# Kernel optimization log

Measured on AMD Instinct MI355X. Metric: run time of the kernel, lower is better.

Reference implementation:

```python
import jax, jax.numpy as jnp
import numpy as np

B, C, I = 4096, 256, 16          # nodes, channels (num_features), per-channel irrep dim (lmax=3)
K3, K2, K1 = 23, 4, 1            # num symmetric-contraction paths per correlation order


def setup_inputs() -> dict:
    key = jax.random.key(0)
    ks = jax.random.split(key, 8)
    return {
        "node_feats": jax.random.normal(ks[0], (B, C, I), jnp.float32),
        "U3": jax.random.normal(ks[1], (I, I, I, K3), jnp.float32),  # fixed CG basis, corr=3
        "U2": jax.random.normal(ks[2], (I, I, K2), jnp.float32),     # fixed CG basis, corr=2
        "U1": jax.random.normal(ks[3], (I, K1), jnp.float32),        # fixed CG basis, corr=1
        "w3": jax.random.normal(ks[4], (C, K3), jnp.float32),        # per-channel weights, corr=3
        "w2": jax.random.normal(ks[5], (C, K2), jnp.float32),
        "w1": jax.random.normal(ks[6], (C, K1), jnp.float32),
        "W_lin": jax.random.normal(ks[7], (C, C), jnp.float32),      # o3.Linear (scalars) weight
    }


def reference(node_feats, U3, U2, U1, w3, w2, w1, W_lin):
    """MACE symmetric contraction (ProductBasisBlock), vectorized over channels.

    Per-channel math (correlation = 3):
      out = einsum('pqik,k,bi->bpq', U3, w3[c], x[:,c])          # main
      c2  = einsum('pqk,k->pq', U2, w2[c]); out = einsum('bpi,bi->bp', c2+out, x[:,c])
      c1  = einsum('pk,k->p',  U1, w1[c]); out = einsum('bi,bi->b',  c1+out, x[:,c])
    The Python-level per-channel loop is replaced by a channel axis c in the einsums.
    """
    x = node_feats                                            # (B, C, I)
    # --- main contraction at correlation order 3 ---
    U3w = jnp.einsum('pqik,ck->cpqi', U3, w3)                 # (C, I, I, I)
    out = jnp.einsum('cpqi,bci->bcpq', U3w, x)                # (B, C, I, I)
    # --- corr = 2 ---
    c2 = jnp.einsum('pik,ck->cpi', U2, w2)                    # (C, I, I)
    out = jnp.einsum('bcpi,bci->bcp', c2[None] + out, x)      # (B, C, I)
    # --- corr = 1 ---
    c1 = jnp.einsum('ik,ck->ci', U1, w1)                      # (C, I)
    out = jnp.einsum('bci,bci->bc', c1[None] + out, x)        # (B, C)
    # --- o3.Linear on the scalar (0e) outputs: x @ W with 1/sqrt(fan_in) path norm ---
    inv_sqrt_fan_in = 1.0 / np.sqrt(C).astype(np.float32)
    return jnp.einsum('bc,cd->bd', out, W_lin) * inv_sqrt_fan_in
```

## Files before the change

kernel.cpp:

```cpp
#include <hip/hip_runtime.h>


#define B_NODES 4096
#define C_CH    256
#define K3      23
#define K2      4

#define KSTEPS   7
#define KB_ELEMS (KSTEPS * 64 * 8)
#define KB_U32   (KB_ELEMS / 2)

#define TILES_PER_WAVE 8

typedef short    short8 __attribute__((ext_vector_type(8)));
typedef float    f32x4  __attribute__((ext_vector_type(4)));
typedef unsigned u32x4  __attribute__((ext_vector_type(4)));

static constexpr size_t OFF_BF_BYTES = 0;
static constexpr size_t OFF_ST_BYTES = (size_t)C_CH * KB_ELEMS * 2;

__device__ inline unsigned short f2bf_rne(float f) {
  unsigned u = __builtin_bit_cast(unsigned, f);
  unsigned r = u + 0x7FFFu + ((u >> 16) & 1u);
  return (unsigned short)(r >> 16);
}

#define F2U(f) __builtin_bit_cast(unsigned, (f))
#define PK2(YH, YL) __builtin_amdgcn_perm(F2U(YH), F2U(YL), 0x07060302u)

__global__ __launch_bounds__(256) void precompute_bfrag(
    const float* __restrict__ U3, const float* __restrict__ U2,
    const float* __restrict__ U1, const float* __restrict__ w3,
    const float* __restrict__ w2, const float* __restrict__ w1,
    unsigned int* __restrict__ bfrag_u32) {
  const int c = blockIdx.x;
  const int t = threadIdx.x;

  __shared__ float su3w[4096];
  for (int l = t; l < 4096; l += 256) {
    float a = 0.f;
#pragma unroll
    for (int k3 = 0; k3 < K3; ++k3)
      a += U3[(size_t)l * K3 + k3] * w3[c * K3 + k3];
    su3w[l] = a;
  }
  __syncthreads();

  const int lane = t >> 2;
  const int jj   = (t & 3) * 2;
  const int p = lane & 15, g = lane >> 4;

#pragma unroll
  for (int s = 0; s < 4; ++s) {
    const int q = 2 * s + (g >> 1);
    float v0 = 0.f, v1 = 0.f;
#pragma unroll
    for (int e = 0; e < 2; ++e) {
      const int i = (g & 1) * 8 + jj + e;
      float a = 0.f;
      if (q < i)
        a = su3w[(p * 16 + q) * 16 + i] + su3w[(p * 16 + i) * 16 + q];
      else if (q == i)
        a = su3w[(p * 16 + q) * 16 + q];
      if (e == 0) v0 = a; else v1 = a;
    }
    bfrag_u32[(size_t)c * KB_U32 + s * 256 + t] =
        (unsigned)f2bf_rne(v0) | ((unsigned)f2bf_rne(v1) << 16);
  }

#pragma unroll
  for (int s = 4; s < 6; ++s) {
    const int q = 8 + (s - 4) * 4 + g;
    float v0 = 0.f, v1 = 0.f;
#pragma unroll
    for (int e = 0; e < 2; ++e) {
      const int i = 8 + jj + e;
      float a = 0.f;
      if (q < i)
        a = su3w[(p * 16 + q) * 16 + i] + su3w[(p * 16 + i) * 16 + q];
      else if (q == i)
        a = su3w[(p * 16 + q) * 16 + q];
      if (e == 0) v0 = a; else v1 = a;
    }
    bfrag_u32[(size_t)c * KB_U32 + s * 256 + t] =
        (unsigned)f2bf_rne(v0) | ((unsigned)f2bf_rne(v1) << 16);
  }

  {
    float v0 = 0.f, v1 = 0.f;
#pragma unroll
    for (int e = 0; e < 2; ++e) {
      const int k = 256 + g * 8 + jj + e;
      float a = 0.f;
      if (k < 272) {
        const int q = k - 256;
#pragma unroll
        for (int k2 = 0; k2 < K2; ++k2)
          a += U2[(size_t)(p * 16 + q) * K2 + k2] * w2[c * K2 + k2];
      } else if (k == 272) {
        a = U1[p] * w1[c];
      }
      if (e == 0) v0 = a; else v1 = a;
    }
    bfrag_u32[(size_t)c * KB_U32 + 6 * 256 + t] =
        (unsigned)f2bf_rne(v0) | ((unsigned)f2bf_rne(v1) << 16);
  }
}


#define QSTEP8(BF, XQ, H0, H1, H2, H3, H4, H5, H6, H7, ACC)                    \
  __builtin_amdgcn_mfma_f32_16x16x32_bf16((BF),                                \
      __builtin_bit_cast(short8, (u32x4){                                      \
          PK2((XQ) * (H1), (XQ) * (H0)), PK2((XQ) * (H3), (XQ) * (H2)),        \
          PK2((XQ) * (H5), (XQ) * (H4)), PK2((XQ) * (H7), (XQ) * (H6))}),      \
      (ACC), 0, 0, 0)

#define TILE_BODY(X0, X1, X2, X3, Tc)                                          \
  do {                                                                         \
    const float xh0 = ghi ? (X2).x : (X0).x;                                   \
    const float xh1 = ghi ? (X2).y : (X0).y;                                   \
    const float xh2 = ghi ? (X2).z : (X0).z;                                   \
    const float xh3 = ghi ? (X2).w : (X0).w;                                   \
    const float xh4 = ghi ? (X3).x : (X1).x;                                   \
    const float xh5 = ghi ? (X3).y : (X1).y;                                   \
    const float xh6 = ghi ? (X3).z : (X1).z;                                   \
    const float xh7 = ghi ? (X3).w : (X1).w;                                   \
    const float xq0 = gq ? (X0).y : (X0).x;                                    \
    const float xq1 = gq ? (X0).w : (X0).z;                                    \
    const float xq2 = gq ? (X1).y : (X1).x;                                    \
    const float xq3 = gq ? (X1).w : (X1).z;                                    \
    const float xq4 = (g == 0) ? (X2).x                                        \
                   : (g == 1) ? (X2).y                                         \
                   : (g == 2) ? (X2).z : (X2).w;                  \
    const float xq5 = (g == 0) ? (X3).x                                        \
                   : (g == 1) ? (X3).y                                         \
                   : (g == 2) ? (X3).z : (X3).w;                  \
    f32x4 acc  = (f32x4){0.f, 0.f, 0.f, 0.f};                                  \
    f32x4 acc2 = (f32x4){0.f, 0.f, 0.f, 0.f};                                  \
    acc  = QSTEP8(bf0, xq0, xh0, xh1, xh2, xh3, xh4, xh5, xh6, xh7, acc);      \
    acc2 = QSTEP8(bf1, xq1, xh0, xh1, xh2, xh3, xh4, xh5, xh6, xh7, acc2);     \
    acc  = QSTEP8(bf2, xq2, xh0, xh1, xh2, xh3, xh4, xh5, xh6, xh7, acc);      \
    acc2 = QSTEP8(bf3, xq3, xh0, xh1, xh2, xh3, xh4, xh5, xh6, xh7, acc2);     \
    acc  = QSTEP8(bf4, xq4, (X2).x, (X2).y, (X2).z, (X2).w,                    \
                  (X3).x, (X3).y, (X3).z, (X3).w, acc);                        \
    acc2 = QSTEP8(bf5, xq5, (X2).x, (X2).y, (X2).z, (X2).w,                    \
                  (X3).x, (X3).y, (X3).z, (X3).w, acc2);                       \
    {                                                                          \
      const float y0 = glin ? xh0 : cst;                                       \
      const float y1 = glin ? xh1 : 0.f;                                       \
      const float y2 = glin ? xh2 : 0.f;                                       \
      const float y3 = glin ? xh3 : 0.f;                                       \
      const float y4 = glin ? xh4 : 0.f;                                       \
      const float y5 = glin ? xh5 : 0.f;                                       \
      const float y6 = glin ? xh6 : 0.f;                                       \
      const float y7 = glin ? xh7 : 0.f;                                       \
      acc = __builtin_amdgcn_mfma_f32_16x16x32_bf16(bf6,                       \
          __builtin_bit_cast(short8, (u32x4){PK2(y1, y0), PK2(y3, y2),         \
                                             PK2(y5, y4), PK2(y7, y6)}),       \
          acc, 0, 0, 0);                                                       \
    }                                                                          \
    acc = acc + acc2;                                                          \
    const float4 xs = (g & 2) ? ((g & 1) ? (X3) : (X2))                        \
                              : ((g & 1) ? (X1) : (X0));                       \
    float v = acc[0] * xs.x + acc[1] * xs.y + acc[2] * xs.z + acc[3] * xs.w;   \
    v += __shfl_xor(v, 16);                                                    \
    v += __shfl_xor(v, 32);                                                    \
    if (g == 0) sTrow[(Tc) * 16 + n] = v;                                      \
  } while (0)

__global__ __launch_bounds__(256)
__attribute__((amdgpu_waves_per_eu(2, 4)))
void contract_mfma(
    const float* __restrict__ x, const short8* __restrict__ bfragv,
    float* __restrict__ sT) {
  const int c0  = blockIdx.x * 4;
  const int nb0 = blockIdx.y * (TILES_PER_WAVE * 16);
  const int t   = threadIdx.x;
  const int w = t >> 6, lane = t & 63, n = lane & 15, g = lane >> 4;
  const int ch = c0 + w;

  const short8* bp = bfragv + (size_t)ch * (KSTEPS * 64);
  const short8 bf0 = bp[0 * 64 + lane];
  const short8 bf1 = bp[1 * 64 + lane];
  const short8 bf2 = bp[2 * 64 + lane];
  const short8 bf3 = bp[3 * 64 + lane];
  const short8 bf4 = bp[4 * 64 + lane];
  const short8 bf5 = bp[5 * 64 + lane];
  const short8 bf6 = bp[6 * 64 + lane];

  const bool  ghi  = (g & 1) != 0;
  const bool  gq   = ((g >> 1) & 1) != 0;
  const bool  glin = (g < 2);
  const float cst  = (g == 2) ? 1.0f : 0.0f;
  float* sTrow = sT + (size_t)ch * B_NODES + nb0;

  const float* xb = x + (size_t)(nb0 + n) * (C_CH * 16) + (size_t)ch * 16;
  const size_t tstride = (size_t)16 * C_CH * 16;

  float4 a0, a1, a2, a3, b0, b1, b2, b3;
  {
    const float4* p = (const float4*)xb;
    a0 = p[0]; a1 = p[1]; a2 = p[2]; a3 = p[3];
  }

#pragma unroll
  for (int TT = 0; TT < TILES_PER_WAVE / 2; ++TT) {
    {
      const float4* p = (const float4*)(xb + (size_t)(2 * TT + 1) * tstride);
      b0 = p[0]; b1 = p[1]; b2 = p[2]; b3 = p[3];
    }
    TILE_BODY(a0, a1, a2, a3, 2 * TT);
    if (TT + 1 < TILES_PER_WAVE / 2) {
      const float4* p = (const float4*)(xb + (size_t)(2 * TT + 2) * tstride);
      a0 = p[0]; a1 = p[1]; a2 = p[2]; a3 = p[3];
    }
    TILE_BODY(b0, b1, b2, b3, 2 * TT + 1);
  }
}

__global__ __launch_bounds__(256) void linear_kernel(
    const float* __restrict__ sT, const float* __restrict__ W,
    float* __restrict__ out) {
  const int b0 = blockIdx.x * 64;
  const int d0 = blockIdx.y * 64;
  const int t  = threadIdx.x;
  const int tx = t & 15;
  const int ty = t >> 4;

  __shared__ float As[16][64];
  __shared__ float Bs[16][64];
  float acc[4][4] = {};

  for (int k0 = 0; k0 < C_CH; k0 += 16) {
    const int kk  = t >> 6;
    const int col = t & 63;
#pragma unroll
    for (int r = 0; r < 4; ++r) {
      As[kk + r * 4][col] = sT[(size_t)(k0 + kk + r * 4) * B_NODES + b0 + col];
      Bs[kk + r * 4][col] = W[(size_t)(k0 + kk + r * 4) * C_CH + d0 + col];
    }
    __syncthreads();
#pragma unroll
    for (int k = 0; k < 16; ++k) {
      float a[4], bv[4];
#pragma unroll
      for (int i = 0; i < 4; ++i) a[i] = As[k][ty * 4 + i];
#pragma unroll
      for (int j = 0; j < 4; ++j) bv[j] = Bs[k][tx * 4 + j];
#pragma unroll
      for (int i = 0; i < 4; ++i)
#pragma unroll
        for (int j = 0; j < 4; ++j) acc[i][j] += a[i] * bv[j];
    }
    __syncthreads();
  }

#pragma unroll
  for (int i = 0; i < 4; ++i) {
    float4 v = make_float4(acc[i][0] * 0.0625f, acc[i][1] * 0.0625f,
                           acc[i][2] * 0.0625f, acc[i][3] * 0.0625f);
    *(float4*)(out + (size_t)(b0 + ty * 4 + i) * C_CH + d0 + tx * 4) = v;
  }
}

extern "C" void kernel_launch(void* const* d_in, const int* in_sizes, int n_in,
                              void* d_out, int out_size, void* d_ws, size_t ws_size,
                              hipStream_t stream) {
  const float* x  = (const float*)d_in[0];
  const float* U3 = (const float*)d_in[1];
  const float* U2 = (const float*)d_in[2];
  const float* U1 = (const float*)d_in[3];
  const float* w3 = (const float*)d_in[4];
  const float* w2 = (const float*)d_in[5];
  const float* w1 = (const float*)d_in[6];
  const float* Wl = (const float*)d_in[7];

  unsigned int* bfrag = (unsigned int*)((char*)d_ws + OFF_BF_BYTES);
  float*        sT    = (float*)((char*)d_ws + OFF_ST_BYTES);
  float*        out   = (float*)d_out;

  precompute_bfrag<<<dim3(C_CH), dim3(256), 0, stream>>>(
      U3, U2, U1, w3, w2, w1, bfrag);
  contract_mfma<<<dim3(C_CH / 4, B_NODES / (TILES_PER_WAVE * 16)), dim3(256), 0, stream>>>(
      x, (const short8*)bfrag, sT);
  linear_kernel<<<dim3(B_NODES / 64, C_CH / 64), dim3(256), 0, stream>>>(sT, Wl, out);
}
```

Baseline: 151.3 us.

## Stage node-feature tiles into LDS via async global_load_lds with swizzle

The contraction kernel now issues all eight per-wave tile loads up front as direct global-to-LDS 16-byte transfers, using an XOR-swizzled layout. Each tile is processed after a staged s_waitcnt vmcnt that counts down the outstanding loads. Per-tile results are held in registers and written once at the end. The aim is deeper memory-level parallelism and coalesced loads, in place of the per-lane strided float4 register double-buffer, at the cost of extra LDS usage and LDS read traffic.

```diff
diff --git a/kernel.cpp b/kernel.cpp
--- a/kernel.cpp
+++ b/kernel.cpp
@@ -27,6 +27,12 @@
 
 #define F2U(f) __builtin_bit_cast(unsigned, (f))
 #define PK2(YH, YL) __builtin_amdgcn_perm(F2U(YH), F2U(YL), 0x07060302u)
+
+__device__ __forceinline__ void stage16(const float* g, float* l) {
+  __builtin_amdgcn_global_load_lds(
+      (const __attribute__((address_space(1))) unsigned int*)g,
+      (__attribute__((address_space(3))) unsigned int*)l, 16, 0, 0);
+}
 
 __global__ __launch_bounds__(256) void precompute_bfrag(
     const float* __restrict__ U3, const float* __restrict__ U2,
@@ -115,7 +121,7 @@
           PK2((XQ) * (H5), (XQ) * (H4)), PK2((XQ) * (H7), (XQ) * (H6))}),      \
       (ACC), 0, 0, 0)
 
-#define TILE_BODY(X0, X1, X2, X3, Tc)                                          \
+#define TILE_BODY(X0, X1, X2, X3, VOUT)                                        \
   do {                                                                         \
     const float xh0 = ghi ? (X2).x : (X0).x;                                   \
     const float xh1 = ghi ? (X2).y : (X0).y;                                   \
@@ -160,12 +166,24 @@
           acc, 0, 0, 0);                                                       \
     }                                                                          \
     acc = acc + acc2;                                                          \
-    const float4 xs = (g & 2) ? ((g & 1) ? (X3) : (X2))                        \
-                              : ((g & 1) ? (X1) : (X0));                       \
-    float v = acc[0] * xs.x + acc[1] * xs.y + acc[2] * xs.z + acc[3] * xs.w;   \
+    const float4 xs4 = (g & 2) ? ((g & 1) ? (X3) : (X2))                       \
+                               : ((g & 1) ? (X1) : (X0));                      \
+    float v = acc[0] * xs4.x + acc[1] * xs4.y + acc[2] * xs4.z + acc[3] * xs4.w;\
     v += __shfl_xor(v, 16);                                                    \
     v += __shfl_xor(v, 32);                                                    \
-    if (g == 0) sTrow[(Tc) * 16 + n] = v;                                      \
+    (VOUT) = v;                                                                \
+  } while (0)
+
+#define TILE_AT(T, NREM, VOUT)                                                 \
+  do {                                                                         \
+    asm volatile("s_waitcnt vmcnt(" #NREM ")" ::: "memory");                   \
+    __builtin_amdgcn_sched_barrier(0);                                         \
+    const float* lw = lbase + (T) * 256;                                       \
+    const float4 X0 = *(const float4*)(lw + n16 + sw0);                        \
+    const float4 X1 = *(const float4*)(lw + n16 + sw1);                        \
+    const float4 X2 = *(const float4*)(lw + n16 + sw2);                        \
+    const float4 X3 = *(const float4*)(lw + n16 + sw3);                        \
+    TILE_BODY(X0, X1, X2, X3, VOUT);                                           \
   } while (0)
 
 __global__ __launch_bounds__(256)
@@ -179,6 +197,8 @@
   const int w = t >> 6, lane = t & 63, n = lane & 15, g = lane >> 4;
   const int ch = c0 + w;
 
+  __shared__ float xstage[4][TILES_PER_WAVE][256];
+
   const short8* bp = bfragv + (size_t)ch * (KSTEPS * 64);
   const short8 bf0 = bp[0 * 64 + lane];
   const short8 bf1 = bp[1 * 64 + lane];
@@ -194,27 +214,44 @@
   const float cst  = (g == 2) ? 1.0f : 0.0f;
   float* sTrow = sT + (size_t)ch * B_NODES + nb0;
 
-  const float* xb = x + (size_t)(nb0 + n) * (C_CH * 16) + (size_t)ch * 16;
+  const int nl = lane >> 2;
+  const int sl = lane & 3;
+  const int cg = sl ^ ((nl >> 1) & 3);
   const size_t tstride = (size_t)16 * C_CH * 16;
-
-  float4 a0, a1, a2, a3, b0, b1, b2, b3;
-  {
-    const float4* p = (const float4*)xb;
-    a0 = p[0]; a1 = p[1]; a2 = p[2]; a3 = p[3];
-  }
-
-#pragma unroll
-  for (int TT = 0; TT < TILES_PER_WAVE / 2; ++TT) {
-    {
-      const float4* p = (const float4*)(xb + (size_t)(2 * TT + 1) * tstride);
-      b0 = p[0]; b1 = p[1]; b2 = p[2]; b3 = p[3];
-    }
-    TILE_BODY(a0, a1, a2, a3, 2 * TT);
-    if (TT + 1 < TILES_PER_WAVE / 2) {
-      const float4* p = (const float4*)(xb + (size_t)(2 * TT + 2) * tstride);
-      a0 = p[0]; a1 = p[1]; a2 = p[2]; a3 = p[3];
-    }
-    TILE_BODY(b0, b1, b2, b3, 2 * TT + 1);
+  const float* gs = x + (size_t)(nb0 + nl) * (C_CH * 16) + (size_t)ch * 16
+                      + (size_t)cg * 4;
+  float* lbase = &xstage[w][0][0];
+#pragma unroll
+  for (int T = 0; T < TILES_PER_WAVE; ++T)
+    stage16(gs + (size_t)T * tstride, lbase + T * 256);
+  __builtin_amdgcn_sched_barrier(0);
+
+  const int n16 = n * 16;
+  const int swz = (n >> 1) & 3;
+  const int sw0 = (0 ^ swz) << 2;
+  const int sw1 = (1 ^ swz) << 2;
+  const int sw2 = (2 ^ swz) << 2;
+  const int sw3 = (3 ^ swz) << 2;
+
+  float v0, v1, v2, v3, v4, v5, v6, v7;
+  TILE_AT(0, 7, v0);
+  TILE_AT(1, 6, v1);
+  TILE_AT(2, 5, v2);
+  TILE_AT(3, 4, v3);
+  TILE_AT(4, 3, v4);
+  TILE_AT(5, 2, v5);
+  TILE_AT(6, 1, v6);
+  TILE_AT(7, 0, v7);
+
+  if (g == 0) {
+    sTrow[0 * 16 + n] = v0;
+    sTrow[1 * 16 + n] = v1;
+    sTrow[2 * 16 + n] = v2;
+    sTrow[3 * 16 + n] = v3;
+    sTrow[4 * 16 + n] = v4;
+    sTrow[5 * 16 + n] = v5;
+    sTrow[6 * 16 + n] = v6;
+    sTrow[7 * 16 + n] = v7;
   }
 }
 
```

Result: faster. 138.6 us (-8.4%).
